# Performance work log

Measured on AMD Instinct MI355X. Metric: run time of the kernel, lower is better.

The kernel has to match this reference:

```python
import jax, jax.numpy as jnp
import numpy as np

DIM = 1024
DEPTH = 2
D_STATE = 16
EXPAND = 2            # standard Mamba expand factor -> d_inner = 2*dim
D_CONV = 4
DT_RANK = DIM // 16   # ceil(dim/16) = 64
D_INNER = DIM * EXPAND
BATCH = 2
SEQ = 1024


def setup_inputs() -> dict:
    key = jax.random.key(0)
    ks = jax.random.split(key, 8)
    def n(k, shape, scale):
        return jax.random.normal(k, shape, jnp.float32) * scale
    # A_log initialized as log(1..N) per channel (S4D-real init, as in mamba_ssm)
    A_log = jnp.tile(jnp.log(jnp.arange(1, D_STATE + 1, dtype=jnp.float32))[None, None, :],
                     (DEPTH, D_INNER, 1))
    return {
        "x": n(ks[0], (BATCH, SEQ, DIM), 1.0),
        "in_proj_w": n(ks[1], (DEPTH, 2 * D_INNER, DIM), DIM ** -0.5),
        "conv_w": n(ks[2], (DEPTH, D_INNER, D_CONV), D_CONV ** -0.5),
        "conv_b": jnp.zeros((DEPTH, D_INNER), jnp.float32),
        "x_proj_w": n(ks[3], (DEPTH, DT_RANK + 2 * D_STATE, D_INNER), D_INNER ** -0.5),
        "dt_proj_w": n(ks[4], (DEPTH, D_INNER, DT_RANK), DT_RANK ** -0.5),
        "dt_proj_b": n(ks[5], (DEPTH, D_INNER), 0.1),
        "A_log": A_log,
        "D": jnp.ones((DEPTH, D_INNER), jnp.float32),
        "out_proj_w": n(ks[6], (DEPTH, DIM, D_INNER), D_INNER ** -0.5),
    }


def _mamba_layer(x, in_w, cw, cb, xp_w, dtw, dtb, A_log, Dp, ow):
    # x: [B, L, dim]
    Bsz = x.shape[0]
    xz = jnp.einsum('bld,ed->ble', x, in_w)            # [B, L, 2*d_inner]
    xi, z = jnp.split(xz, 2, axis=-1)
    # causal depthwise conv1d over time
    xc = jnp.transpose(xi, (0, 2, 1))                  # [B, d_inner, L]
    xc = jax.lax.conv_general_dilated(xc, cw[:, None, :], (1,), [(D_CONV - 1, 0)],
                                      feature_group_count=D_INNER)
    xc = xc + cb[None, :, None]
    xc = jax.nn.silu(jnp.transpose(xc, (0, 2, 1)))     # [B, L, d_inner]
    # input-dependent dt, B, C
    x_dbl = jnp.einsum('bld,ed->ble', xc, xp_w)        # [B, L, dt_rank+2*N]
    dt_raw = x_dbl[..., :DT_RANK]
    Bm = x_dbl[..., DT_RANK:DT_RANK + D_STATE]         # [B, L, N]
    Cm = x_dbl[..., DT_RANK + D_STATE:]                # [B, L, N]
    dt = jax.nn.softplus(jnp.einsum('blr,dr->bld', dt_raw, dtw) + dtb)  # [B, L, d_inner]
    A = -jnp.exp(A_log)                                # [d_inner, N]
    dA = jnp.exp(dt[..., None] * A[None, None])        # [B, L, d_inner, N]
    dBu = dt[..., None] * Bm[:, :, None, :] * xc[..., None]

    def step(h, inp):
        dA_t, dBu_t, C_t = inp
        h = dA_t * h + dBu_t                           # [B, d_inner, N]
        y = jnp.einsum('bdn,bn->bd', h, C_t)
        return h, y

    h0 = jnp.zeros((Bsz, D_INNER, D_STATE), x.dtype)
    _, ys = jax.lax.scan(step, h0,
                         (dA.transpose(1, 0, 2, 3), dBu.transpose(1, 0, 2, 3),
                          Cm.transpose(1, 0, 2)))
    y = ys.transpose(1, 0, 2) + Dp[None, None, :] * xc
    y = y * jax.nn.silu(z)
    return jnp.einsum('bld,od->blo', y, ow)


def reference(x, in_proj_w, conv_w, conv_b, x_proj_w, dt_proj_w, dt_proj_b, A_log, D, out_proj_w):
    for i in range(DEPTH):
        x = _mamba_layer(x, in_proj_w[i], conv_w[i], conv_b[i], x_proj_w[i],
                         dt_proj_w[i], dt_proj_b[i], A_log[i], D[i], out_proj_w[i])
    return x
```

## Files before the change

### kernel.cpp

```cpp
#include <hip/hip_runtime.h>
#include <hip/hip_bf16.h>

typedef __hip_bfloat16 bf16;
typedef __attribute__((ext_vector_type(8))) short short8;
typedef __attribute__((ext_vector_type(4))) short shortx4;
typedef __attribute__((ext_vector_type(4))) float floatx4;

#define BATCH   2
#define SEQ     1024
#define DIM     1024
#define D_INNER 2048
#define D_STATE 16
#define DT_RANK 64
#define MROWS   (BATCH * SEQ)
#define CHUNK   32
#define NCHUNK  (SEQ / CHUNK)

__device__ __forceinline__ float bf2f(bf16 x) { return __bfloat162float(x); }
__device__ __forceinline__ bf16  f2bf(float x) { return __float2bfloat16(x); }
__device__ __forceinline__ short bfbits(float x) {
    bf16 b = __float2bfloat16(x); short s; __builtin_memcpy(&s, &b, 2); return s;
}

__device__ __forceinline__ void ld_lds16(const void* g, void* l) {
    __builtin_amdgcn_global_load_lds(
        (const __attribute__((address_space(1))) void*)g,
        (__attribute__((address_space(3))) void*)l, 16, 0, 0);
}

__global__ __launch_bounds__(256) void cast_k(
    const float* __restrict__ in, short* __restrict__ o, int n4)
{
    int i = blockIdx.x * 256 + threadIdx.x;
    if (i >= n4) return;
    floatx4 v = ((const floatx4*)in)[i];
    shortx4 r;
    r.x = bfbits(v.x); r.y = bfbits(v.y); r.z = bfbits(v.z); r.w = bfbits(v.w);
    ((shortx4*)o)[i] = r;
}

__device__ __forceinline__ short8 ld8_any(const void* p, size_t eoff, int is_f32) {
    if (is_f32) {
        const float* f = (const float*)p + eoff;
        floatx4 a = *(const floatx4*)f;
        floatx4 b = *(const floatx4*)(f + 4);
        short8 r;
        r[0] = bfbits(a[0]); r[1] = bfbits(a[1]); r[2] = bfbits(a[2]); r[3] = bfbits(a[3]);
        r[4] = bfbits(b[0]); r[5] = bfbits(b[1]); r[6] = bfbits(b[2]); r[7] = bfbits(b[3]);
        return r;
    } else {
        return *(const short8*)((const bf16*)p + eoff);
    }
}

__global__ __launch_bounds__(256) void gemm128(
    const bf16* __restrict__ A, int lda,
    const bf16* __restrict__ B, int ldb,
    float* __restrict__ Cf, bf16* __restrict__ Cb, int ldc,
    int kchunk, size_t psize)
{
    __shared__ short As[128 * 32];
    __shared__ short Bs[128 * 32];
    const int tid  = threadIdx.x;
    const int wave = tid >> 6;
    const int lane = tid & 63;
    const int m0 = blockIdx.y * 128;
    const int n0 = blockIdx.x * 128;
    const int wm = (wave & 1) * 64;
    const int wn = (wave >> 1) * 64;
    const int r16  = lane & 15;
    const int quad = lane >> 4;
    const int r0 = tid >> 2;
    const int c0 = (tid & 3) << 3;
    const int kbeg = blockIdx.z * kchunk;

    floatx4 acc[4][4] = {};

    for (int k0 = kbeg; k0 < kbeg + kchunk; k0 += 32) {
        __syncthreads();
        ld_lds16(A + (size_t)(m0 + r0) * lda + k0 + c0,      As + tid * 8);
        ld_lds16(A + (size_t)(m0 + r0 + 64) * lda + k0 + c0, As + (tid + 256) * 8);
        ld_lds16(B + (size_t)(n0 + r0) * ldb + k0 + c0,      Bs + tid * 8);
        ld_lds16(B + (size_t)(n0 + r0 + 64) * ldb + k0 + c0, Bs + (tid + 256) * 8);
        __syncthreads();
        short8 af[4], bg[4];
#pragma unroll
        for (int i = 0; i < 4; i++) {
            af[i] = *(const short8*)(As + (wm + i * 16 + r16) * 32 + quad * 8);
            bg[i] = *(const short8*)(Bs + (wn + i * 16 + r16) * 32 + quad * 8);
        }
#pragma unroll
        for (int i = 0; i < 4; i++)
#pragma unroll
            for (int j = 0; j < 4; j++)
                acc[i][j] = __builtin_amdgcn_mfma_f32_16x16x32_bf16(af[i], bg[j], acc[i][j], 0, 0, 0);
    }

    float* Cfp = Cf ? Cf + (size_t)blockIdx.z * psize : nullptr;
#pragma unroll
    for (int i = 0; i < 4; i++)
#pragma unroll
        for (int j = 0; j < 4; j++) {
            int gm = m0 + wm + i * 16 + quad * 4;
            int gn = n0 + wn + j * 16 + r16;
#pragma unroll
            for (int r = 0; r < 4; r++) {
                size_t o = (size_t)(gm + r) * ldc + gn;
                float v = acc[i][j][r];
                if (Cfp) Cfp[o] = v;
                if (Cb) Cb[o] = f2bf(v);
            }
        }
}

__global__ __launch_bounds__(256) void gemm_bt(
    const void* __restrict__ A, int a_f32, int lda,
    const void* __restrict__ B, int b_f32, int ldb,
    float* __restrict__ Cf, bf16* __restrict__ Cb, int ldc,
    int N, int K, size_t psize,
    const float* __restrict__ bias, int act)
{
    __shared__ short As[64][40];
    __shared__ short Bs[64][40];
    const int m0   = blockIdx.y * 64;
    const int n0   = blockIdx.x * 64;
    const int tid  = threadIdx.x;
    const int wave = tid >> 6;
    const int lane = tid & 63;
    const int srow = tid >> 2;
    const int scol = (tid & 3) << 3;
    const int r16  = lane & 15;
    const int quad = lane >> 4;
    const int kbeg = blockIdx.z * K;

    floatx4 acc[4] = {};

    for (int k0 = kbeg; k0 < kbeg + K; k0 += 32) {
        short8 av = ld8_any(A, (size_t)(m0 + srow) * lda + k0 + scol, a_f32);
        short8 bv = {};
        int gn = n0 + srow;
        if (gn < N) bv = ld8_any(B, (size_t)gn * ldb + k0 + scol, b_f32);
        *(short8*)(&As[srow][scol]) = av;
        *(short8*)(&Bs[srow][scol]) = bv;
        __syncthreads();
        short8 af = *(const short8*)(&As[wave * 16 + r16][quad * 8]);
#pragma unroll
        for (int nt = 0; nt < 4; nt++) {
            short8 bq = *(const short8*)(&Bs[nt * 16 + r16][quad * 8]);
            acc[nt] = __builtin_amdgcn_mfma_f32_16x16x32_bf16(af, bq, acc[nt], 0, 0, 0);
        }
        __syncthreads();
    }

    float* Cfp = Cf ? Cf + (size_t)blockIdx.z * psize : nullptr;
#pragma unroll
    for (int nt = 0; nt < 4; nt++) {
        int gn = n0 + nt * 16 + r16;
        if (gn >= N) continue;
        float bsv = bias ? bias[gn] : 0.f;
#pragma unroll
        for (int r = 0; r < 4; r++) {
            int gm = m0 + wave * 16 + quad * 4 + r;
            float v = acc[nt][r] + bsv;
            if (act == 1) v = (v > 20.f) ? v : log1pf(__expf(v));
            size_t o = (size_t)gm * ldc + gn;
            if (Cfp) Cfp[o] = v;
            if (Cb) Cb[o] = f2bf(v);
        }
    }
}

__global__ __launch_bounds__(256) void reduce4_k(
    const float* __restrict__ part, float* __restrict__ o, int n, size_t psize)
{
    int i = blockIdx.x * 256 + threadIdx.x;
    if (i < n)
        o[i] = part[i] + part[i + psize] + part[i + 2 * psize] + part[i + 3 * psize];
}

__global__ __launch_bounds__(256) void reduce2_k(
    const float* __restrict__ part, size_t psize, int n,
    float* __restrict__ of, bf16* __restrict__ ob)
{
    int i = blockIdx.x * 256 + threadIdx.x;
    if (i >= n) return;
    float v = part[i] + part[i + psize];
    if (of) of[i] = v;
    if (ob) ob[i] = f2bf(v);
}

__global__ __launch_bounds__(256) void conv_silu_k(
    const bf16* __restrict__ xz, const float* __restrict__ cw,
    const float* __restrict__ cb, bf16* __restrict__ xcb)
{
    int idx = blockIdx.x * 256 + threadIdx.x;
    int d   = idx & (D_INNER - 1);
    int bt  = idx >> 11;
    int t   = bt & (SEQ - 1);
    float s = cb[d];
#pragma unroll
    for (int j = 0; j < 4; j++) {
        int tt = t - 3 + j;
        if (tt >= 0) s += cw[d * 4 + j] * bf2f(xz[(size_t)(bt - 3 + j) * 4096 + d]);
    }
    float sig = 1.f / (1.f + __expf(-s));
    xcb[idx] = f2bf(s * sig);
}

__global__ __launch_bounds__(256) void scan1_k(
    const float* __restrict__ dtf, const bf16* __restrict__ xcb,
    const float* __restrict__ xdbl, const float* __restrict__ Alog,
    float* __restrict__ chunk_sdt, float* __restrict__ chunk_S)
{
    __shared__ float dt_s[CHUNK][256];
    __shared__ short xc_s[CHUNK][256];
    __shared__ float B_s[CHUNK][16];
    const int tid = threadIdx.x;
    const int d0  = blockIdx.x * 256;
    const int d   = d0 + tid;
    const int b   = blockIdx.y;
    const int c   = blockIdx.z;
    const size_t rbase = (size_t)b * SEQ + c * CHUNK;

#pragma unroll 4
    for (int t = 0; t < CHUNK; t++) {
        dt_s[t][tid] = dtf[(rbase + t) * D_INNER + d0 + tid];
        ((short*)xc_s)[t * 256 + tid] = *(const short*)&xcb[(rbase + t) * D_INNER + d0 + tid];
    }
    for (int e = tid; e < CHUNK * 16; e += 256) {
        int t = e >> 4, n = e & 15;
        B_s[t][n] = xdbl[(rbase + t) * 96 + 64 + n];
    }
    float A[16];
#pragma unroll
    for (int n = 0; n < 16; n++) A[n] = -__expf(Alog[(size_t)d * 16 + n]);
    float h[16] = {};
    float sdt = 0.f;
    __syncthreads();

    for (int t = 0; t < CHUNK; t++) {
        float dtv = dt_s[t][tid];
        bf16 xcr; short xs = xc_s[t][tid]; __builtin_memcpy(&xcr, &xs, 2);
        float u = dtv * bf2f(xcr);
        sdt += dtv;
        floatx4 B0 = *(const floatx4*)&B_s[t][0];
        floatx4 B1 = *(const floatx4*)&B_s[t][4];
        floatx4 B2 = *(const floatx4*)&B_s[t][8];
        floatx4 B3 = *(const floatx4*)&B_s[t][12];
#pragma unroll
        for (int n = 0; n < 4; n++) {
            h[n]      = __expf(dtv * A[n])      * h[n]      + u * B0[n];
            h[n + 4]  = __expf(dtv * A[n + 4])  * h[n + 4]  + u * B1[n];
            h[n + 8]  = __expf(dtv * A[n + 8])  * h[n + 8]  + u * B2[n];
            h[n + 12] = __expf(dtv * A[n + 12]) * h[n + 12] + u * B3[n];
        }
    }
    chunk_sdt[(b * NCHUNK + c) * D_INNER + d] = sdt;
#pragma unroll
    for (int n = 0; n < 16; n++)
        chunk_S[((size_t)(b * NCHUNK + c) * 16 + n) * D_INNER + d] = h[n];
}

__global__ __launch_bounds__(256) void scan2_k(
    const float* __restrict__ dtf, const bf16* __restrict__ xcb,
    const float* __restrict__ xdbl, const bf16* __restrict__ xz,
    const float* __restrict__ Alog, const float* __restrict__ Dp,
    const float* __restrict__ chunk_sdt, const float* __restrict__ chunk_S,
    bf16* __restrict__ yb)
{
    __shared__ float dt_s[CHUNK][256];
    __shared__ short xc_s[CHUNK][256];
    __shared__ float B_s[CHUNK][16];
    __shared__ float C_s[CHUNK][16];
    const int tid = threadIdx.x;
    const int d0  = blockIdx.x * 256;
    const int d   = d0 + tid;
    const int b   = blockIdx.y;
    const int c   = blockIdx.z;
    const size_t rbase = (size_t)b * SEQ + c * CHUNK;

#pragma unroll 4
    for (int t = 0; t < CHUNK; t++) {
        dt_s[t][tid] = dtf[(rbase + t) * D_INNER + d0 + tid];
        ((short*)xc_s)[t * 256 + tid] = *(const short*)&xcb[(rbase + t) * D_INNER + d0 + tid];
    }
    for (int e = tid; e < CHUNK * 16; e += 256) {
        int t = e >> 4, n = e & 15;
        B_s[t][n] = xdbl[(rbase + t) * 96 + 64 + n];
        C_s[t][n] = xdbl[(rbase + t) * 96 + 80 + n];
    }
    float A[16];
#pragma unroll
    for (int n = 0; n < 16; n++) A[n] = -__expf(Alog[(size_t)d * 16 + n]);

    float h[16] = {};
    for (int j = 0; j < c; j++) {
        float sdt = chunk_sdt[(b * NCHUNK + j) * D_INNER + d];
#pragma unroll
        for (int n = 0; n < 16; n++) {
            float S = chunk_S[((size_t)(b * NCHUNK + j) * 16 + n) * D_INNER + d];
            h[n] = __expf(sdt * A[n]) * h[n] + S;
        }
    }
    const float Dv = Dp[d];
    __syncthreads();

    for (int t = 0; t < CHUNK; t++) {
        size_t row = rbase + t;
        float dtv = dt_s[t][tid];
        bf16 xcr; short xs = xc_s[t][tid]; __builtin_memcpy(&xcr, &xs, 2);
        float xcv = bf2f(xcr);
        float u = dtv * xcv;
        floatx4 B0 = *(const floatx4*)&B_s[t][0];
        floatx4 B1 = *(const floatx4*)&B_s[t][4];
        floatx4 B2 = *(const floatx4*)&B_s[t][8];
        floatx4 B3 = *(const floatx4*)&B_s[t][12];
        floatx4 C0 = *(const floatx4*)&C_s[t][0];
        floatx4 C1 = *(const floatx4*)&C_s[t][4];
        floatx4 C2 = *(const floatx4*)&C_s[t][8];
        floatx4 C3 = *(const floatx4*)&C_s[t][12];
        float y = 0.f;
#pragma unroll
        for (int n = 0; n < 4; n++) {
            h[n]      = __expf(dtv * A[n])      * h[n]      + u * B0[n];
            h[n + 4]  = __expf(dtv * A[n + 4])  * h[n + 4]  + u * B1[n];
            h[n + 8]  = __expf(dtv * A[n + 8])  * h[n + 8]  + u * B2[n];
            h[n + 12] = __expf(dtv * A[n + 12]) * h[n + 12] + u * B3[n];
            y += h[n] * C0[n] + h[n + 4] * C1[n] + h[n + 8] * C2[n] + h[n + 12] * C3[n];
        }
        float zv = bf2f(xz[row * 4096 + 2048 + d]);
        y = (y + Dv * xcv) * (zv / (1.f + __expf(-zv)));
        yb[row * D_INNER + d] = f2bf(y);
    }
}

extern "C" void kernel_launch(void* const* d_in, const int* in_sizes, int n_in,
                              void* d_out, int out_size, void* d_ws, size_t ws_size,
                              hipStream_t stream)
{
    const float* x    = (const float*)d_in[0];
    const float* inw  = (const float*)d_in[1];
    const float* cw   = (const float*)d_in[2];
    const float* cb   = (const float*)d_in[3];
    const float* xpw  = (const float*)d_in[4];
    const float* dtw  = (const float*)d_in[5];
    const float* dtb  = (const float*)d_in[6];
    const float* Alog = (const float*)d_in[7];
    const float* Dp   = (const float*)d_in[8];
    const float* ow   = (const float*)d_in[9];
    float* out = (float*)d_out;

    char* p = (char*)d_ws;
    bf16*  xzb   = (bf16*)p;  p += (size_t)MROWS * 4096 * 2;
    bf16*  xcb   = (bf16*)p;  p += (size_t)MROWS * D_INNER * 2;
    float* xdblf = (float*)p; p += (size_t)MROWS * 96 * 4;
    float* dtf   = (float*)p; p += (size_t)MROWS * D_INNER * 4;
    bf16*  ybf   = (bf16*)p;  p += (size_t)MROWS * D_INNER * 2;
    bf16*  xmid  = (bf16*)p;  p += (size_t)MROWS * DIM * 2;
    float* csdt  = (float*)p; p += (size_t)BATCH * NCHUNK * D_INNER * 4;
    float* cS    = (float*)p; p += (size_t)BATCH * NCHUNK * 16 * D_INNER * 4;
    bf16*  xb    = (bf16*)p;  p += (size_t)MROWS * DIM * 2;
    bf16*  inwb  = (bf16*)p;  p += (size_t)2 * D_INNER * DIM * 2;
    bf16*  owb   = (bf16*)p;  p += (size_t)DIM * D_INNER * 2;
    float* xprt  = (float*)p; p += (size_t)4 * MROWS * 96 * 4;

    const size_t xp_psize = (size_t)MROWS * 96;
    const size_t op_psize = (size_t)MROWS * DIM;
    float* outp = dtf;

    cast_k<<<(MROWS * DIM / 4 + 255) / 256, 256, 0, stream>>>(x, (short*)xb, MROWS * DIM / 4);

    for (int l = 0; l < 2; l++) {
        const float* xpw_l = xpw + (size_t)l * 96 * D_INNER;
        const float* dtw_l = dtw + (size_t)l * D_INNER * DT_RANK;
        const float* Al    = Alog + (size_t)l * D_INNER * D_STATE;

        cast_k<<<(2 * D_INNER * DIM / 4 + 255) / 256, 256, 0, stream>>>(
            inw + (size_t)l * 2 * D_INNER * DIM, (short*)inwb, 2 * D_INNER * DIM / 4);
        cast_k<<<(DIM * D_INNER / 4 + 255) / 256, 256, 0, stream>>>(
            ow + (size_t)l * DIM * D_INNER, (short*)owb, DIM * D_INNER / 4);

        gemm128<<<dim3(32, 16, 1), 256, 0, stream>>>(
            (l == 0) ? xb : xmid, DIM, inwb, DIM,
            nullptr, xzb, 4096, DIM, 0);

        conv_silu_k<<<(MROWS * D_INNER) / 256, 256, 0, stream>>>(
            xzb, cw + (size_t)l * D_INNER * 4, cb + (size_t)l * D_INNER, xcb);

        gemm_bt<<<dim3(2, 32, 4), 256, 0, stream>>>(
            xcb, 0, D_INNER, xpw_l, 1, D_INNER,
            xprt, nullptr, 96, 96, 512, xp_psize, nullptr, 0);
        reduce4_k<<<(MROWS * 96 + 255) / 256, 256, 0, stream>>>(
            xprt, xdblf, MROWS * 96, xp_psize);

        gemm_bt<<<dim3(32, 32), 256, 0, stream>>>(
            xdblf, 1, 96, dtw_l, 1, DT_RANK,
            dtf, nullptr, D_INNER, D_INNER, DT_RANK, 0,
            dtb + (size_t)l * D_INNER, 1);

        scan1_k<<<dim3(D_INNER / 256, BATCH, NCHUNK), 256, 0, stream>>>(
            dtf, xcb, xdblf, Al, csdt, cS);
        scan2_k<<<dim3(D_INNER / 256, BATCH, NCHUNK), 256, 0, stream>>>(
            dtf, xcb, xdblf, xzb, Al, Dp + (size_t)l * D_INNER,
            csdt, cS, ybf);

        gemm128<<<dim3(8, 16, 2), 256, 0, stream>>>(
            ybf, D_INNER, owb, D_INNER,
            outp, nullptr, DIM, D_INNER / 2, op_psize);
        reduce2_k<<<(MROWS * DIM + 255) / 256, 256, 0, stream>>>(
            outp, op_psize, MROWS * DIM,
            (l == 1) ? out : nullptr, (l == 0) ? xmid : nullptr);
    }
}
```

Measured before the change: 473.3 us.

## Add chunk-prefix scan kernel, fuse weight casts, widen x_proj split-K

A new scanpre_k kernel computes the inter-chunk state prefix once per (batch, channel, state), so scan2 only loads its starting state instead of each chunk redoing an O(c) recurrence over all earlier chunks. The two weight-cast launches are merged into one kernel. The x_proj GEMM split-K goes from 4 to 8 slices, with a matching 8-way reduce. The extra launch and the larger partial buffer are the cost, traded for removing quadratic work in scan2 and raising parallelism in the skinny GEMM.

```diff
diff --git a/kernel.cpp b/kernel.cpp
--- a/kernel.cpp
+++ b/kernel.cpp
@@ -28,15 +28,25 @@
         (__attribute__((address_space(3))) void*)l, 16, 0, 0);
 }
 
-__global__ __launch_bounds__(256) void cast_k(
-    const float* __restrict__ in, short* __restrict__ o, int n4)
-{
-    int i = blockIdx.x * 256 + threadIdx.x;
-    if (i >= n4) return;
+__device__ __forceinline__ void cast4(const float* in, short* o, int i) {
     floatx4 v = ((const floatx4*)in)[i];
     shortx4 r;
     r.x = bfbits(v.x); r.y = bfbits(v.y); r.z = bfbits(v.z); r.w = bfbits(v.w);
     ((shortx4*)o)[i] = r;
+}
+__global__ __launch_bounds__(256) void cast_k(
+    const float* __restrict__ in, short* __restrict__ o, int n4)
+{
+    int i = blockIdx.x * 256 + threadIdx.x;
+    if (i < n4) cast4(in, o, i);
+}
+__global__ __launch_bounds__(256) void cast2_k(
+    const float* __restrict__ a, short* __restrict__ oa, int na4,
+    const float* __restrict__ b, short* __restrict__ ob, int nb4)
+{
+    int i = blockIdx.x * 256 + threadIdx.x;
+    if (i < na4) cast4(a, oa, i);
+    else if (i - na4 < nb4) cast4(b, ob, i - na4);
 }
 
 __device__ __forceinline__ short8 ld8_any(const void* p, size_t eoff, int is_f32) {
@@ -170,12 +180,15 @@
     }
 }
 
-__global__ __launch_bounds__(256) void reduce4_k(
+__global__ __launch_bounds__(256) void reduce8_k(
     const float* __restrict__ part, float* __restrict__ o, int n, size_t psize)
 {
     int i = blockIdx.x * 256 + threadIdx.x;
-    if (i < n)
-        o[i] = part[i] + part[i + psize] + part[i + 2 * psize] + part[i + 3 * psize];
+    if (i >= n) return;
+    float v = 0.f;
+#pragma unroll
+    for (int j = 0; j < 8; j++) v += part[i + (size_t)j * psize];
+    o[i] = v;
 }
 
 __global__ __launch_bounds__(256) void reduce2_k(
@@ -261,12 +274,29 @@
         chunk_S[((size_t)(b * NCHUNK + c) * 16 + n) * D_INNER + d] = h[n];
 }
 
+__global__ __launch_bounds__(256) void scanpre_k(
+    const float* __restrict__ Alog, const float* __restrict__ chunk_sdt,
+    float* __restrict__ chunk_S)
+{
+    const int d = blockIdx.x * 256 + threadIdx.x;
+    const int b = blockIdx.y;
+    const int n = blockIdx.z;
+    const float Av = -__expf(Alog[(size_t)d * 16 + n]);
+    float h = 0.f;
+    for (int j = 0; j < NCHUNK; j++) {
+        size_t si = ((size_t)(b * NCHUNK + j) * 16 + n) * D_INNER + d;
+        float S   = chunk_S[si];
+        float sdt = chunk_sdt[(b * NCHUNK + j) * D_INNER + d];
+        chunk_S[si] = h;
+        h = __expf(sdt * Av) * h + S;
+    }
+}
+
 __global__ __launch_bounds__(256) void scan2_k(
     const float* __restrict__ dtf, const bf16* __restrict__ xcb,
     const float* __restrict__ xdbl, const bf16* __restrict__ xz,
     const float* __restrict__ Alog, const float* __restrict__ Dp,
-    const float* __restrict__ chunk_sdt, const float* __restrict__ chunk_S,
-    bf16* __restrict__ yb)
+    const float* __restrict__ chunk_S, bf16* __restrict__ yb)
 {
     __shared__ float dt_s[CHUNK][256];
     __shared__ short xc_s[CHUNK][256];
@@ -293,15 +323,11 @@
 #pragma unroll
     for (int n = 0; n < 16; n++) A[n] = -__expf(Alog[(size_t)d * 16 + n]);
 
-    float h[16] = {};
-    for (int j = 0; j < c; j++) {
-        float sdt = chunk_sdt[(b * NCHUNK + j) * D_INNER + d];
-#pragma unroll
-        for (int n = 0; n < 16; n++) {
-            float S = chunk_S[((size_t)(b * NCHUNK + j) * 16 + n) * D_INNER + d];
-            h[n] = __expf(sdt * A[n]) * h[n] + S;
-        }
-    }
+    float h[16];
+#pragma unroll
+    for (int n = 0; n < 16; n++)
+        h[n] = chunk_S[((size_t)(b * NCHUNK + c) * 16 + n) * D_INNER + d];
+
     const float Dv = Dp[d];
     __syncthreads();
 
@@ -362,7 +388,7 @@
     bf16*  xb    = (bf16*)p;  p += (size_t)MROWS * DIM * 2;
     bf16*  inwb  = (bf16*)p;  p += (size_t)2 * D_INNER * DIM * 2;
     bf16*  owb   = (bf16*)p;  p += (size_t)DIM * D_INNER * 2;
-    float* xprt  = (float*)p; p += (size_t)4 * MROWS * 96 * 4;
+    float* xprt  = (float*)p; p += (size_t)8 * MROWS * 96 * 4;
 
     const size_t xp_psize = (size_t)MROWS * 96;
     const size_t op_psize = (size_t)MROWS * DIM;
@@ -375,10 +401,12 @@
         const float* dtw_l = dtw + (size_t)l * D_INNER * DT_RANK;
         const float* Al    = Alog + (size_t)l * D_INNER * D_STATE;
 
-        cast_k<<<(2 * D_INNER * DIM / 4 + 255) / 256, 256, 0, stream>>>(
-            inw + (size_t)l * 2 * D_INNER * DIM, (short*)inwb, 2 * D_INNER * DIM / 4);
-        cast_k<<<(DIM * D_INNER / 4 + 255) / 256, 256, 0, stream>>>(
-            ow + (size_t)l * DIM * D_INNER, (short*)owb, DIM * D_INNER / 4);
+        {
+            int na4 = 2 * D_INNER * DIM / 4, nb4 = DIM * D_INNER / 4;
+            cast2_k<<<(na4 + nb4 + 255) / 256, 256, 0, stream>>>(
+                inw + (size_t)l * 2 * D_INNER * DIM, (short*)inwb, na4,
+                ow + (size_t)l * DIM * D_INNER, (short*)owb, nb4);
+        }
 
         gemm128<<<dim3(32, 16, 1), 256, 0, stream>>>(
             (l == 0) ? xb : xmid, DIM, inwb, DIM,
@@ -387,10 +415,10 @@
         conv_silu_k<<<(MROWS * D_INNER) / 256, 256, 0, stream>>>(
             xzb, cw + (size_t)l * D_INNER * 4, cb + (size_t)l * D_INNER, xcb);
 
-        gemm_bt<<<dim3(2, 32, 4), 256, 0, stream>>>(
+        gemm_bt<<<dim3(2, 32, 8), 256, 0, stream>>>(
             xcb, 0, D_INNER, xpw_l, 1, D_INNER,
-            xprt, nullptr, 96, 96, 512, xp_psize, nullptr, 0);
-        reduce4_k<<<(MROWS * 96 + 255) / 256, 256, 0, stream>>>(
+            xprt, nullptr, 96, 96, 256, xp_psize, nullptr, 0);
+        reduce8_k<<<(MROWS * 96 + 255) / 256, 256, 0, stream>>>(
             xprt, xdblf, MROWS * 96, xp_psize);
 
         gemm_bt<<<dim3(32, 32), 256, 0, stream>>>(
@@ -400,9 +428,10 @@
 
         scan1_k<<<dim3(D_INNER / 256, BATCH, NCHUNK), 256, 0, stream>>>(
             dtf, xcb, xdblf, Al, csdt, cS);
+        scanpre_k<<<dim3(D_INNER / 256, BATCH, D_STATE), 256, 0, stream>>>(
+            Al, csdt, cS);
         scan2_k<<<dim3(D_INNER / 256, BATCH, NCHUNK), 256, 0, stream>>>(
-            dtf, xcb, xdblf, xzb, Al, Dp + (size_t)l * D_INNER,
-            csdt, cS, ybf);
+            dtf, xcb, xdblf, xzb, Al, Dp + (size_t)l * D_INNER, cS, ybf);
 
         gemm128<<<dim3(8, 16, 2), 256, 0, stream>>>(
             ybf, D_INNER, owb, D_INNER,
```

Measured after the change: 445.7 us. 5.8% less time.
